# Kernel optimization log

Hardware: AMD Instinct MI355X
Metric: run time of the kernel (lower is better)

The kernel has to match this reference:

```python
import jax, jax.numpy as jnp
import numpy as np

B, S, DIM = 2, 2048, 2048
H, DH = 16, 128
FF = 4 * DIM
EPS = 1e-5


def layer_norm(x, w, b, eps=EPS):
    m = jnp.mean(x, axis=-1, keepdims=True)
    v = jnp.mean(jnp.square(x - m), axis=-1, keepdims=True)
    return (x - m) * jax.lax.rsqrt(v + eps) * w + b


def apply_rotary(x, cos, sin):
    # x: [B, H, S, DH]; cos/sin: [S, DH//2]; complex multiply on (even, odd) pairs
    x2 = x.reshape(*x.shape[:-1], DH // 2, 2)
    x0, x1 = x2[..., 0], x2[..., 1]
    c = cos[None, None, :, :]
    s = sin[None, None, :, :]
    r0 = x0 * c - x1 * s
    r1 = x0 * s + x1 * c
    return jnp.stack([r0, r1], axis=-1).reshape(x.shape)


def setup_inputs() -> dict:
    key = jax.random.key(0)
    ks = jax.random.split(key, 16)
    sc = 0.02
    pos = jnp.arange(S, dtype=jnp.float32)[:, None]
    inv_freq = 1.0 / (10000.0 ** (jnp.arange(0, DH // 2, dtype=jnp.float32) / (DH // 2)))
    ang = pos * inv_freq[None, :]
    return {
        "hidden_states": jax.random.normal(ks[0], (B, S, DIM), jnp.float32),
        "freqs_cos": jnp.cos(ang),
        "freqs_sin": jnp.sin(ang),
        "wq": jax.random.normal(ks[1], (DIM, H * DH), jnp.float32) * sc,
        "wk": jax.random.normal(ks[2], (DIM, H * DH), jnp.float32) * sc,
        "wv": jax.random.normal(ks[3], (DIM, H * DH), jnp.float32) * sc,
        "nq_w": jnp.ones((DH,), jnp.float32),
        "nq_b": jnp.zeros((DH,), jnp.float32),
        "nk_w": jnp.ones((DH,), jnp.float32),
        "nk_b": jnp.zeros((DH,), jnp.float32),
        "wo": jax.random.normal(ks[4], (H * DH, DIM), jnp.float32) * sc,
        "bo": jnp.zeros((DIM,), jnp.float32),
        "ln1_w": jnp.ones((DIM,), jnp.float32),
        "ln1_b": jnp.zeros((DIM,), jnp.float32),
        "ln3_w": jnp.ones((DIM,), jnp.float32),
        "ln3_b": jnp.zeros((DIM,), jnp.float32),
        "w1": jax.random.normal(ks[5], (DIM, FF), jnp.float32) * sc,
        "b1": jnp.zeros((FF,), jnp.float32),
        "w2": jax.random.normal(ks[6], (FF, DIM), jnp.float32) * sc,
        "b2": jnp.zeros((DIM,), jnp.float32),
    }


def reference(hidden_states, freqs_cos, freqs_sin, wq, wk, wv, nq_w, nq_b, nk_w, nk_b,
              wo, bo, ln1_w, ln1_b, ln3_w, ln3_b, w1, b1, w2, b2):
    x = hidden_states
    # --- self-attention branch ---
    n = layer_norm(x, ln1_w, ln1_b)                       # [B,S,DIM]
    q = (n @ wq).reshape(B, S, H, DH)
    k = (n @ wk).reshape(B, S, H, DH)
    v = (n @ wv).reshape(B, S, H, DH)
    # per-head QK LayerNorm (norm over dim_head)
    q = layer_norm(q, nq_w, nq_b)
    k = layer_norm(k, nk_w, nk_b)
    q = q.transpose(0, 2, 1, 3)                            # [B,H,S,DH]
    k = k.transpose(0, 2, 1, 3)
    v = v.transpose(0, 2, 1, 3)
    q = apply_rotary(q, freqs_cos, freqs_sin)
    k = apply_rotary(k, freqs_cos, freqs_sin)
    scale = DH ** -0.5
    scores = jnp.einsum("bhqd,bhkd->bhqk", q, k) * scale   # [B,H,S,S]
    probs = jax.nn.softmax(scores, axis=-1)
    attn = jnp.einsum("bhqk,bhkd->bhqd", probs, v)         # [B,H,S,DH]
    attn = attn.transpose(0, 2, 1, 3).reshape(B, S, H * DH)
    x = x + (attn @ wo + bo)
    # --- feed-forward branch ---
    n = layer_norm(x, ln3_w, ln3_b)
    h = jax.nn.gelu(n @ w1 + b1, approximate=False)
    x = x + (h @ w2 + b2)
    return x
```

## Files before the change

### kernel.cpp

```cpp
#include <hip/hip_runtime.h>
#include <hip/hip_bf16.h>
#include <stdint.h>

typedef __hip_bfloat16 bf16;
typedef float v4f __attribute__((ext_vector_type(4)));
typedef short v8s __attribute__((ext_vector_type(8)));

#define DEV __device__ __forceinline__

DEV float b2f(bf16 x) { return __bfloat162float(x); }
DEV bf16 f2b(float x) { return __float2bfloat16(x); }

DEV void load4(const float* p, float* f) {
  float4 t = *(const float4*)p;
  f[0] = t.x; f[1] = t.y; f[2] = t.z; f[3] = t.w;
}
DEV void load4(const bf16* p, float* f) {
  union { uint2 u; bf16 h[4]; } t;
  t.u = *(const uint2*)p;
#pragma unroll
  for (int i = 0; i < 4; i++) f[i] = b2f(t.h[i]);
}
DEV void load8(const float* p, float* f) {
  float4 a = ((const float4*)p)[0], b = ((const float4*)p)[1];
  f[0] = a.x; f[1] = a.y; f[2] = a.z; f[3] = a.w;
  f[4] = b.x; f[5] = b.y; f[6] = b.z; f[7] = b.w;
}
DEV void load8(const bf16* p, float* f) {
  union { uint4 u; bf16 h[8]; } t;
  t.u = *(const uint4*)p;
#pragma unroll
  for (int i = 0; i < 8; i++) f[i] = b2f(t.h[i]);
}
DEV void store4(bf16* p, const float* f) {
  union { uint2 u; bf16 h[4]; } t;
#pragma unroll
  for (int i = 0; i < 4; i++) t.h[i] = f2b(f[i]);
  *(uint2*)p = t.u;
}
DEV void store4(float* p, const float* f) {
  *(float4*)p = make_float4(f[0], f[1], f[2], f[3]);
}

DEV void gld_lds16(const bf16* g, bf16* l) {
  auto gp = reinterpret_cast<const __attribute__((address_space(1))) uint32_t*>(
      reinterpret_cast<uintptr_t>(g));
  auto lp = reinterpret_cast<__attribute__((address_space(3))) uint32_t*>(
      reinterpret_cast<uintptr_t>(l));
  __builtin_amdgcn_global_load_lds(gp, lp, 16, 0, 0);
}

template <typename XT>
__global__ __launch_bounds__(256)
void ln2048_kernel(const XT* __restrict__ x, const float* __restrict__ w,
                   const float* __restrict__ b, bf16* __restrict__ y) {
  const int N = 2048;
  int row = blockIdx.x, tid = threadIdx.x;
  const XT* xr = x + (size_t)row * N;
  bf16* yr = y + (size_t)row * N;
  float f[8], s = 0.f, ss = 0.f;
  load8(xr + tid * 8, f);
#pragma unroll
  for (int i = 0; i < 8; i++) { s += f[i]; ss += f[i] * f[i]; }
#pragma unroll
  for (int off = 32; off >= 1; off >>= 1) {
    s  += __shfl_xor(s, off, 64);
    ss += __shfl_xor(ss, off, 64);
  }
  __shared__ float red0[4], red1[4];
  int wv = tid >> 6;
  if ((tid & 63) == 0) { red0[wv] = s; red1[wv] = ss; }
  __syncthreads();
  s  = red0[0] + red0[1] + red0[2] + red0[3];
  ss = red1[0] + red1[1] + red1[2] + red1[3];
  float mean = s * (1.f / N);
  float var  = ss * (1.f / N) - mean * mean;
  float inv  = rsqrtf(var + 1e-5f);
  float wf[8], bf_[8];
  load8(w + tid * 8, wf);
  load8(b + tid * 8, bf_);
  union { uint4 u; bf16 h[8]; } vo;
#pragma unroll
  for (int i = 0; i < 8; i++)
    vo.h[i] = f2b((f[i] - mean) * inv * wf[i] + bf_[i]);
  ((uint4*)yr)[tid] = vo.u;
}

__global__ __launch_bounds__(256)
void headln_rope_kernel(bf16* __restrict__ q, const float* __restrict__ w,
                        const float* __restrict__ b, const float* __restrict__ fcos,
                        const float* __restrict__ fsin) {
  int tid = threadIdx.x;
  int wv = tid >> 6, ln = tid & 63;
  int idx = blockIdx.x * 4 + wv;
  int row = idx >> 4, h = idx & 15;
  int srow = row & 2047;
  bf16* p = q + (size_t)row * 2048 + h * 128 + ln * 2;
  union { unsigned int u; bf16 h2[2]; } v;
  v.u = *(const unsigned int*)p;
  float x0 = b2f(v.h2[0]), x1 = b2f(v.h2[1]);
  float s = x0 + x1, ss = x0 * x0 + x1 * x1;
#pragma unroll
  for (int off = 32; off >= 1; off >>= 1) {
    s  += __shfl_xor(s, off, 64);
    ss += __shfl_xor(ss, off, 64);
  }
  float mean = s * (1.f / 128.f);
  float var  = ss * (1.f / 128.f) - mean * mean;
  float inv  = rsqrtf(var + 1e-5f);
  float w0 = w[ln * 2], w1 = w[ln * 2 + 1];
  float b0 = b[ln * 2], b1 = b[ln * 2 + 1];
  x0 = (x0 - mean) * inv * w0 + b0;
  x1 = (x1 - mean) * inv * w1 + b1;
  float c  = fcos[srow * 64 + ln];
  float sn = fsin[srow * 64 + ln];
  v.h2[0] = f2b(x0 * c - x1 * sn);
  v.h2[1] = f2b(x0 * sn + x1 * c);
  *(unsigned int*)p = v.u;
}

__global__ __launch_bounds__(256)
void convT_kernel(const float* __restrict__ src, bf16* __restrict__ dst,
                  int K, int N) {
  __shared__ float T[64][65];
  int n0 = blockIdx.x * 64, k0 = blockIdx.y * 64;
  int t = threadIdx.x;
  int tr = t >> 4, tc4 = (t & 15) * 4;
#pragma unroll
  for (int it = 0; it < 4; it++) {
    float4 v = *(const float4*)&src[(size_t)(k0 + tr + 16 * it) * N + n0 + tc4];
    T[tr + 16 * it][tc4 + 0] = v.x;
    T[tr + 16 * it][tc4 + 1] = v.y;
    T[tr + 16 * it][tc4 + 2] = v.z;
    T[tr + 16 * it][tc4 + 3] = v.w;
  }
  __syncthreads();
#pragma unroll
  for (int it = 0; it < 4; it++) {
    int n = tr + 16 * it;
    union { uint2 u; bf16 h[4]; } o;
#pragma unroll
    for (int c = 0; c < 4; c++) o.h[c] = f2b(T[tc4 + c][n]);
    *(uint2*)&dst[(size_t)(n0 + n) * K + k0 + tc4] = o.u;
  }
}

template <int EPI, typename RT, typename OT>
__global__ __launch_bounds__(256, 2)
void mfma_gemm_kernel(const bf16* __restrict__ A, const bf16* __restrict__ BT,
                      OT* __restrict__ C, const float* __restrict__ bias,
                      const RT* __restrict__ res, int M, int N, int K) {
  __shared__ __align__(16) bf16 As[128 * 32];
  __shared__ __align__(16) bf16 Bs[128 * 32];
  int tid = threadIdx.x;
  int lane = tid & 63, wave = tid >> 6;
  int wr = wave >> 1, wc = wave & 1;
  int m0 = blockIdx.y * 128, n0 = blockIdx.x * 128;

  int ls_row = lane >> 2;
  int ls_k   = (lane & 3) * 8;
  int t0 = 2 * wave, t1 = 2 * wave + 1;
  const bf16* gA0 = A  + (size_t)(m0 + 16 * t0 + ls_row) * K + ls_k;
  const bf16* gA1 = A  + (size_t)(m0 + 16 * t1 + ls_row) * K + ls_k;
  const bf16* gB0 = BT + (size_t)(n0 + 16 * t0 + ls_row) * K + ls_k;
  const bf16* gB1 = BT + (size_t)(n0 + 16 * t1 + ls_row) * K + ls_k;
  bf16* lA0 = As + t0 * 512;
  bf16* lA1 = As + t1 * 512;
  bf16* lB0 = Bs + t0 * 512;
  bf16* lB1 = Bs + t1 * 512;

  int fr = lane & 15, fk = (lane >> 4) * 8;
  const bf16* pA = As + (wr * 64 + fr) * 32 + fk;
  const bf16* pB = Bs + (wc * 64 + fr) * 32 + fk;

  v4f acc[4][4];
#pragma unroll
  for (int i = 0; i < 4; i++)
#pragma unroll
    for (int j = 0; j < 4; j++) acc[i][j] = (v4f){0.f, 0.f, 0.f, 0.f};

  for (int k0 = 0; k0 < K; k0 += 32) {
    __syncthreads();
    gld_lds16(gA0, lA0); gld_lds16(gA1, lA1);
    gld_lds16(gB0, lB0); gld_lds16(gB1, lB1);
    gA0 += 32; gA1 += 32; gB0 += 32; gB1 += 32;
    __syncthreads();
    v8s af[4], bfr[4];
#pragma unroll
    for (int i = 0; i < 4; i++) af[i]  = *(const v8s*)(pA + i * 16 * 32);
#pragma unroll
    for (int j = 0; j < 4; j++) bfr[j] = *(const v8s*)(pB + j * 16 * 32);
#pragma unroll
    for (int i = 0; i < 4; i++)
#pragma unroll
      for (int j = 0; j < 4; j++)
        acc[i][j] = __builtin_amdgcn_mfma_f32_16x16x32_bf16(af[i], bfr[j],
                                                            acc[i][j], 0, 0, 0);
  }

  int rq = (lane >> 4) * 4;
#pragma unroll
  for (int j = 0; j < 4; j++) {
    int n = n0 + wc * 64 + j * 16 + (lane & 15);
    float bb = (EPI >= 1) ? bias[n] : 0.f;
#pragma unroll
    for (int i = 0; i < 4; i++) {
#pragma unroll
      for (int r = 0; r < 4; r++) {
        int m = m0 + wr * 64 + i * 16 + rq + r;
        float val = acc[i][j][r] + bb;
        if (EPI == 2)
          val = 0.5f * val * (1.f + erff(val * 0.70710678118654752f));
        if (EPI == 1) {
          if constexpr (__is_same(RT, float)) val += res[(size_t)m * N + n];
          else                                val += b2f(res[(size_t)m * N + n]);
        }
        if constexpr (__is_same(OT, float)) C[(size_t)m * N + n] = val;
        else                                C[(size_t)m * N + n] = f2b(val);
      }
    }
  }
}

template <int EPI, typename RT, typename OT>
__global__ __launch_bounds__(256)
void gemm_kernel(const bf16* __restrict__ A, const float* __restrict__ Bm,
                 OT* __restrict__ C, const float* __restrict__ bias,
                 const RT* __restrict__ res, int M, int N, int K) {
  const int BK = 32;
  __shared__ __align__(16) float As[BK][68];
  __shared__ __align__(16) float Bs[BK][68];
  int tid = threadIdx.x;
  int bm = blockIdx.y, bn = blockIdx.x;
  int tx = tid & 15, ty = tid >> 4;
  int am = tid >> 2, ak8 = (tid & 3) * 8;
  int bkr = tid >> 3, bn8 = (tid & 7) * 8;
  const bf16* Aptr = A + (size_t)(bm * 64 + am) * K + ak8;
  const float* Bptr = Bm + (size_t)bkr * N + bn * 64 + bn8;
  float acc[4][4] = {};
  for (int k0 = 0; k0 < K; k0 += BK) {
    float av[8], bv[8];
    load8(Aptr, av);
    load8(Bptr, bv);
    __syncthreads();
#pragma unroll
    for (int j = 0; j < 8; j++) As[ak8 + j][am] = av[j];
#pragma unroll
    for (int j = 0; j < 8; j++) Bs[bkr][bn8 + j] = bv[j];
    __syncthreads();
    Aptr += BK;
    Bptr += (size_t)BK * N;
#pragma unroll 8
    for (int kk = 0; kk < BK; kk++) {
      float a0[4], b0[4];
      *(float4*)a0 = *(const float4*)&As[kk][ty * 4];
      *(float4*)b0 = *(const float4*)&Bs[kk][tx * 4];
#pragma unroll
      for (int i = 0; i < 4; i++)
#pragma unroll
        for (int j = 0; j < 4; j++)
          acc[i][j] += a0[i] * b0[j];
    }
  }
  int m0 = bm * 64 + ty * 4, n0 = bn * 64 + tx * 4;
#pragma unroll
  for (int i = 0; i < 4; i++) {
    float r4[4];
#pragma unroll
    for (int j = 0; j < 4; j++) r4[j] = acc[i][j];
    if (EPI >= 1) {
      float bb[4];
      load4(bias + n0, bb);
#pragma unroll
      for (int j = 0; j < 4; j++) r4[j] += bb[j];
    }
    if (EPI == 2) {
#pragma unroll
      for (int j = 0; j < 4; j++)
        r4[j] = 0.5f * r4[j] * (1.f + erff(r4[j] * 0.70710678118654752f));
    }
    if (EPI == 1) {
      float rr[4];
      load4(res + (size_t)(m0 + i) * N + n0, rr);
#pragma unroll
      for (int j = 0; j < 4; j++) r4[j] += rr[j];
    }
    store4(&C[(size_t)(m0 + i) * N + n0], r4);
  }
}

#define VSWZ(r) (((((r) >> 3) ^ (r)) & 7) << 4)

__global__ __launch_bounds__(256, 2)
void attn_kernel(const bf16* __restrict__ q, const bf16* __restrict__ k,
                 const bf16* __restrict__ v, bf16* __restrict__ o) {
  const int S = 2048, HD = 2048;
  __shared__ __align__(16) char smem[57856];
  char* Ks0 = smem;
  char* Ks1 = smem + 16384;
  char* VtB = smem + 32768;
  char* PB  = smem + 49152;
  float* Lp = (float*)(smem + 57344);

  int id = blockIdx.x;
  int swzb = (id & 7) * 128 + (id >> 3);
  int bh = swzb >> 5, qb = swzb & 31;
  int q0 = qb * 64;
  size_t base = (size_t)(bh >> 4) * S * HD + (size_t)(bh & 15) * 128;

  int tid = threadIdx.x;
  int lane = tid & 63, wave = tid >> 6;
  int wr = wave >> 1, wc = wave & 1;
  int fr = lane & 15, fg = lane >> 4;

  if (tid < 128) Lp[tid] = 0.f;

  union V4U { uint4 u; bf16 h[8]; };
  int vr0 = (tid & 15) * 4, vd0 = (tid >> 4) * 8;

#pragma unroll
  for (int t = 0; t < 4; t++) {
    int ti = wave * 4 + t;
    int r = ti * 4 + fg;
    int cb = (fr * 16) ^ ((r & 7) << 4);
    gld_lds16(q + base + (size_t)(q0 + r) * HD + (cb >> 1), (bf16*)Ks0 + ti * 512);
    gld_lds16(k + base + (size_t)r * HD + (cb >> 1), (bf16*)Ks1 + ti * 512);
  }
  V4U vA[4], vB[4];
#pragma unroll
  for (int j = 0; j < 4; j++)
    vA[j].u = *(const uint4*)&v[base + (size_t)(vr0 + j) * HD + vd0];
  __syncthreads();

  v8s qfrag[2][4];
#pragma unroll
  for (int i = 0; i < 2; i++)
#pragma unroll
    for (int kk = 0; kk < 4; kk++) {
      int row = wr * 32 + i * 16 + fr;
      int off = row * 256 + ((kk * 64 + fg * 16) ^ ((row & 7) << 4));
      qfrag[i][kk] = *(const v8s*)(Ks0 + off);
    }
  __syncthreads();

  v4f oacc[2][4];
#pragma unroll
  for (int i = 0; i < 2; i++)
#pragma unroll
    for (int j = 0; j < 4; j++) oacc[i][j] = (v4f){0.f, 0.f, 0.f, 0.f};

  const float scale = 0.08838834764831845f;

#define ATTN_TILE(KT, KCUR, KNXT, VCUR, VNXT, STAGE_NEXT)                     \
  {                                                                           \
    _Pragma("unroll")                                                         \
    for (int c = 0; c < 8; c++) {                                             \
      int d = vd0 + c;                                                        \
      union { uint2 u2; bf16 hh[4]; } pk;                                     \
      _Pragma("unroll")                                                       \
      for (int j = 0; j < 4; j++) pk.hh[j] = VCUR[j].h[c];                    \
      *(uint2*)(VtB + d * 128 + ((vr0 * 2) ^ VSWZ(d))) = pk.u2;               \
    }                                                                         \
    if (STAGE_NEXT) {                                                         \
      _Pragma("unroll")                                                       \
      for (int t = 0; t < 4; t++) {                                           \
        int ti = wave * 4 + t;                                                \
        int r = ti * 4 + fg;                                                  \
        int cb = (fr * 16) ^ ((r & 7) << 4);                                  \
        gld_lds16(k + base + (size_t)((KT) + 64 + r) * HD + (cb >> 1),        \
                  (bf16*)(KNXT) + ti * 512);                                  \
      }                                                                       \
      _Pragma("unroll")                                                       \
      for (int j = 0; j < 4; j++)                                             \
        VNXT[j].u =                                                           \
            *(const uint4*)&v[base + (size_t)((KT) + 64 + vr0 + j) * HD + vd0]; \
    }                                                                         \
    v4f sacc[2][2];                                                           \
    _Pragma("unroll")                                                         \
    for (int i = 0; i < 2; i++)                                               \
      _Pragma("unroll")                                                       \
      for (int j = 0; j < 2; j++) sacc[i][j] = (v4f){0.f, 0.f, 0.f, 0.f};     \
    __builtin_amdgcn_s_setprio(1);                                            \
    _Pragma("unroll")                                                         \
    for (int kk = 0; kk < 4; kk++) {                                          \
      v8s kf[2];                                                              \
      _Pragma("unroll")                                                       \
      for (int j = 0; j < 2; j++) {                                           \
        int row = wc * 32 + j * 16 + fr;                                      \
        int off = row * 256 + ((kk * 64 + fg * 16) ^ ((row & 7) << 4));       \
        kf[j] = *(const v8s*)((KCUR) + off);                                  \
      }                                                                       \
      _Pragma("unroll")                                                       \
      for (int i = 0; i < 2; i++)                                             \
        _Pragma("unroll")                                                     \
        for (int j = 0; j < 2; j++)                                           \
          sacc[i][j] = __builtin_amdgcn_mfma_f32_16x16x32_bf16(               \
              qfrag[i][kk], kf[j], sacc[i][j], 0, 0, 0);                      \
    }                                                                         \
    __builtin_amdgcn_s_setprio(0);                                            \
    _Pragma("unroll")                                                         \
    for (int i = 0; i < 2; i++)                                               \
      _Pragma("unroll")                                                       \
      for (int r = 0; r < 4; r++) {                                           \
        int qrow = wr * 32 + i * 16 + fg * 4 + r;                             \
        float e0 = __expf(sacc[i][0][r] * scale);                             \
        float e1 = __expf(sacc[i][1][r] * scale);                             \
        int sw = VSWZ(qrow);                                                  \
        int c0 = wc * 64 + fr * 2;                                            \
        *(bf16*)(PB + qrow * 128 + (c0 ^ sw)) = f2b(e0);                      \
        *(bf16*)(PB + qrow * 128 + ((c0 + 32) ^ sw)) = f2b(e1);               \
        float s_ = e0 + e1;                                                   \
        s_ += __shfl_xor(s_, 1, 64);                                          \
        s_ += __shfl_xor(s_, 2, 64);                                          \
        s_ += __shfl_xor(s_, 4, 64);                                          \
        s_ += __shfl_xor(s_, 8, 64);                                          \
        if (fr == 0) Lp[wc * 64 + qrow] += s_;                                \
      }                                                                       \
    __syncthreads();                                                          \
    __builtin_amdgcn_s_setprio(1);                                            \
    _Pragma("unroll")                                                         \
    for (int kk2 = 0; kk2 < 2; kk2++) {                                       \
      v8s pf[2], vf[4];                                                       \
      _Pragma("unroll")                                                       \
      for (int i = 0; i < 2; i++) {                                           \
        int row = wr * 32 + i * 16 + fr;                                      \
        int off = row * 128 + ((kk2 * 64 + fg * 16) ^ VSWZ(row));             \
        pf[i] = *(const v8s*)(PB + off);                                      \
      }                                                                       \
      _Pragma("unroll")                                                       \
      for (int j = 0; j < 4; j++) {                                           \
        int row = wc * 64 + j * 16 + fr;                                      \
        int off = row * 128 + ((kk2 * 64 + fg * 16) ^ VSWZ(row));             \
        vf[j] = *(const v8s*)(VtB + off);                                     \
      }                                                                       \
      _Pragma("unroll")                                                       \
      for (int i = 0; i < 2; i++)                                             \
        _Pragma("unroll")                                                     \
        for (int j = 0; j < 4; j++)                                           \
          oacc[i][j] = __builtin_amdgcn_mfma_f32_16x16x32_bf16(               \
              pf[i], vf[j], oacc[i][j], 0, 0, 0);                             \
    }                                                                         \
    __builtin_amdgcn_s_setprio(0);                                            \
    __syncthreads();                                                          \
  }

  for (int tp = 0; tp < 16; tp++) {
    int kt = tp * 128;
    ATTN_TILE(kt, Ks1, Ks0, vA, vB, true);
    ATTN_TILE(kt + 64, Ks0, Ks1, vB, vA, (tp < 15));
  }
#undef ATTN_TILE

#pragma unroll
  for (int i = 0; i < 2; i++)
#pragma unroll
    for (int r = 0; r < 4; r++) {
      int qrow = wr * 32 + i * 16 + fg * 4 + r;
      float linv = 1.f / (Lp[qrow] + Lp[64 + qrow]);
#pragma unroll
      for (int j = 0; j < 4; j++) {
        int d = wc * 64 + j * 16 + fr;
        o[base + (size_t)(q0 + qrow) * HD + d] = f2b(oacc[i][j][r] * linv);
      }
    }
}

extern "C" void kernel_launch(void* const* d_in, const int* in_sizes, int n_in,
                              void* d_out, int out_size, void* d_ws, size_t ws_size,
                              hipStream_t stream) {
  (void)in_sizes; (void)n_in; (void)out_size;
  const float* x    = (const float*)d_in[0];
  const float* fcos = (const float*)d_in[1];
  const float* fsin = (const float*)d_in[2];
  const float* wq   = (const float*)d_in[3];
  const float* wk   = (const float*)d_in[4];
  const float* wv   = (const float*)d_in[5];
  const float* nqw  = (const float*)d_in[6];
  const float* nqb  = (const float*)d_in[7];
  const float* nkw  = (const float*)d_in[8];
  const float* nkb  = (const float*)d_in[9];
  const float* wo   = (const float*)d_in[10];
  const float* bo   = (const float*)d_in[11];
  const float* ln1w = (const float*)d_in[12];
  const float* ln1b = (const float*)d_in[13];
  const float* ln3w = (const float*)d_in[14];
  const float* ln3b = (const float*)d_in[15];
  const float* w1   = (const float*)d_in[16];
  const float* b1   = (const float*)d_in[17];
  const float* w2   = (const float*)d_in[18];
  const float* b2   = (const float*)d_in[19];
  float* out = (float*)d_out;

  const size_t SEG = (size_t)4096 * 2048;
  bf16* base = (bf16*)d_ws;
  bf16* q        = base + 0 * SEG;
  bf16* k        = base + 1 * SEG;
  bf16* v        = base + 2 * SEG;
  bf16* n1       = base + 3 * SEG;
  bf16* attn_out = base + 3 * SEG;
  bf16* x2       = base + 4 * SEG;
  bf16* n3       = base + 5 * SEG;
  bf16* h        = base + 0 * SEG;

  dim3 blk(256);
  ln2048_kernel<float><<<4096, blk, 0, stream>>>(x, ln1w, ln1b, n1);

  bool mfma_path = ws_size >= (size_t)128 * 1024 * 1024;
  if (mfma_path) {
    bf16* W = base + 6 * SEG;
    bf16* wqT = W;
    bf16* wkT = W + 4 * 1024 * 1024;
    bf16* wvT = W + 8 * 1024 * 1024;
    bf16* woT = W;
    bf16* w1T = W;
    bf16* w2T = W;

    dim3 cg22(32, 32);
    dim3 g16(16, 32);
    dim3 g64(64, 32);

    convT_kernel<<<cg22, blk, 0, stream>>>(wq, wqT, 2048, 2048);
    convT_kernel<<<cg22, blk, 0, stream>>>(wk, wkT, 2048, 2048);
    convT_kernel<<<cg22, blk, 0, stream>>>(wv, wvT, 2048, 2048);
    mfma_gemm_kernel<0, float, bf16><<<g16, blk, 0, stream>>>(n1, wqT, q, nullptr, nullptr, 4096, 2048, 2048);
    mfma_gemm_kernel<0, float, bf16><<<g16, blk, 0, stream>>>(n1, wkT, k, nullptr, nullptr, 4096, 2048, 2048);
    mfma_gemm_kernel<0, float, bf16><<<g16, blk, 0, stream>>>(n1, wvT, v, nullptr, nullptr, 4096, 2048, 2048);
    headln_rope_kernel<<<16384, blk, 0, stream>>>(q, nqw, nqb, fcos, fsin);
    headln_rope_kernel<<<16384, blk, 0, stream>>>(k, nkw, nkb, fcos, fsin);
    attn_kernel<<<1024, blk, 0, stream>>>(q, k, v, attn_out);
    convT_kernel<<<cg22, blk, 0, stream>>>(wo, woT, 2048, 2048);
    mfma_gemm_kernel<1, float, bf16><<<g16, blk, 0, stream>>>(attn_out, woT, x2, bo, x, 4096, 2048, 2048);
    ln2048_kernel<bf16><<<4096, blk, 0, stream>>>(x2, ln3w, ln3b, n3);
    convT_kernel<<<dim3(128, 32), blk, 0, stream>>>(w1, w1T, 2048, 8192);
    mfma_gemm_kernel<2, float, bf16><<<g64, blk, 0, stream>>>(n3, w1T, h, b1, nullptr, 4096, 8192, 2048);
    convT_kernel<<<dim3(32, 128), blk, 0, stream>>>(w2, w2T, 8192, 2048);
    mfma_gemm_kernel<1, bf16, float><<<g16, blk, 0, stream>>>(h, w2T, out, b2, x2, 4096, 2048, 8192);
  } else {
    dim3 g2048(32, 64), g8192(128, 64);
    gemm_kernel<0, float, bf16><<<g2048, blk, 0, stream>>>(n1, wq, q, nullptr, nullptr, 4096, 2048, 2048);
    gemm_kernel<0, float, bf16><<<g2048, blk, 0, stream>>>(n1, wk, k, nullptr, nullptr, 4096, 2048, 2048);
    gemm_kernel<0, float, bf16><<<g2048, blk, 0, stream>>>(n1, wv, v, nullptr, nullptr, 4096, 2048, 2048);
    headln_rope_kernel<<<16384, blk, 0, stream>>>(q, nqw, nqb, fcos, fsin);
    headln_rope_kernel<<<16384, blk, 0, stream>>>(k, nkw, nkb, fcos, fsin);
    attn_kernel<<<1024, blk, 0, stream>>>(q, k, v, attn_out);
    gemm_kernel<1, float, bf16><<<g2048, blk, 0, stream>>>(attn_out, wo, x2, bo, x, 4096, 2048, 2048);
    ln2048_kernel<bf16><<<4096, blk, 0, stream>>>(x2, ln3w, ln3b, n3);
    gemm_kernel<2, float, bf16><<<g8192, blk, 0, stream>>>(n3, w1, h, b1, nullptr, 4096, 8192, 2048);
    gemm_kernel<1, bf16, float><<<g2048, blk, 0, stream>>>(h, w2, out, b2, x2, 4096, 2048, 8192);
  }
}
```

Before: 1.026 ms.

## Fuse QKV projections into one GEMM, merge q/k head-norm launches, swizzle tiles

Runs the Q, K and V projections as a single GEMM with N=6144 over the contiguous transposed weights, and scatters each output column into its separate q/k/v buffer using a segment stride. The two per-head LayerNorm+RoPE launches are merged into one launch that picks q or k by block index. The MFMA GEMM also remaps block IDs in groups of eight to improve L2 reuse. This cuts launch count and tail effects and raises occupancy for the projection, but it assumes wqT/wkT/wvT and q/k/v sit at fixed strides in the workspace.

```diff
diff --git a/kernel.cpp b/kernel.cpp
--- a/kernel.cpp
+++ b/kernel.cpp
@@ -87,15 +87,20 @@
 }
 
 __global__ __launch_bounds__(256)
-void headln_rope_kernel(bf16* __restrict__ q, const float* __restrict__ w,
-                        const float* __restrict__ b, const float* __restrict__ fcos,
-                        const float* __restrict__ fsin) {
+void headln_rope_kernel(bf16* __restrict__ qb, bf16* __restrict__ kb,
+                        const float* __restrict__ nqw, const float* __restrict__ nqb,
+                        const float* __restrict__ nkw, const float* __restrict__ nkb,
+                        const float* __restrict__ fcos, const float* __restrict__ fsin) {
+  int bid = blockIdx.x;
+  bf16* qk; const float* w; const float* b;
+  if (bid < 16384) { qk = qb; w = nqw; b = nqb; }
+  else             { qk = kb; w = nkw; b = nkb; bid -= 16384; }
   int tid = threadIdx.x;
   int wv = tid >> 6, ln = tid & 63;
-  int idx = blockIdx.x * 4 + wv;
+  int idx = bid * 4 + wv;
   int row = idx >> 4, h = idx & 15;
   int srow = row & 2047;
-  bf16* p = q + (size_t)row * 2048 + h * 128 + ln * 2;
+  bf16* p = qk + (size_t)row * 2048 + h * 128 + ln * 2;
   union { unsigned int u; bf16 h2[2]; } v;
   v.u = *(const unsigned int*)p;
   float x0 = b2f(v.h2[0]), x1 = b2f(v.h2[1]);
@@ -149,13 +154,20 @@
 __global__ __launch_bounds__(256, 2)
 void mfma_gemm_kernel(const bf16* __restrict__ A, const bf16* __restrict__ BT,
                       OT* __restrict__ C, const float* __restrict__ bias,
-                      const RT* __restrict__ res, int M, int N, int K) {
+                      const RT* __restrict__ res, int M, int N, int K,
+                      int ldc_log2, size_t seg_stride) {
   __shared__ __align__(16) bf16 As[128 * 32];
   __shared__ __align__(16) bf16 Bs[128 * 32];
   int tid = threadIdx.x;
   int lane = tid & 63, wave = tid >> 6;
   int wr = wave >> 1, wc = wave & 1;
-  int m0 = blockIdx.y * 128, n0 = blockIdx.x * 128;
+
+  int nbx = gridDim.x;
+  int bid = blockIdx.y * nbx + blockIdx.x;
+  int nwg = nbx * gridDim.y;
+  int cpx = nwg >> 3;
+  int swz = (bid & 7) * cpx + (bid >> 3);
+  int m0 = (swz / nbx) * 128, n0 = (swz % nbx) * 128;
 
   int ls_row = lane >> 2;
   int ls_k   = (lane & 3) * 8;
@@ -199,10 +211,12 @@
   }
 
   int rq = (lane >> 4) * 4;
+  int ldm = 1 << ldc_log2;
 #pragma unroll
   for (int j = 0; j < 4; j++) {
     int n = n0 + wc * 64 + j * 16 + (lane & 15);
     float bb = (EPI >= 1) ? bias[n] : 0.f;
+    size_t cseg = (size_t)(n >> ldc_log2) * seg_stride + (n & (ldm - 1));
 #pragma unroll
     for (int i = 0; i < 4; i++) {
 #pragma unroll
@@ -215,8 +229,9 @@
           if constexpr (__is_same(RT, float)) val += res[(size_t)m * N + n];
           else                                val += b2f(res[(size_t)m * N + n]);
         }
-        if constexpr (__is_same(OT, float)) C[(size_t)m * N + n] = val;
-        else                                C[(size_t)m * N + n] = f2b(val);
+        size_t cix = cseg + ((size_t)m << ldc_log2);
+        if constexpr (__is_same(OT, float)) C[cix] = val;
+        else                                C[cix] = f2b(val);
       }
     }
   }
@@ -517,31 +532,28 @@
 
     dim3 cg22(32, 32);
     dim3 g16(16, 32);
+    dim3 g48(48, 32);
     dim3 g64(64, 32);
 
     convT_kernel<<<cg22, blk, 0, stream>>>(wq, wqT, 2048, 2048);
     convT_kernel<<<cg22, blk, 0, stream>>>(wk, wkT, 2048, 2048);
     convT_kernel<<<cg22, blk, 0, stream>>>(wv, wvT, 2048, 2048);
-    mfma_gemm_kernel<0, float, bf16><<<g16, blk, 0, stream>>>(n1, wqT, q, nullptr, nullptr, 4096, 2048, 2048);
-    mfma_gemm_kernel<0, float, bf16><<<g16, blk, 0, stream>>>(n1, wkT, k, nullptr, nullptr, 4096, 2048, 2048);
-    mfma_gemm_kernel<0, float, bf16><<<g16, blk, 0, stream>>>(n1, wvT, v, nullptr, nullptr, 4096, 2048, 2048);
-    headln_rope_kernel<<<16384, blk, 0, stream>>>(q, nqw, nqb, fcos, fsin);
-    headln_rope_kernel<<<16384, blk, 0, stream>>>(k, nkw, nkb, fcos, fsin);
+    mfma_gemm_kernel<0, float, bf16><<<g48, blk, 0, stream>>>(n1, wqT, q, nullptr, nullptr, 4096, 6144, 2048, 11, SEG);
+    headln_rope_kernel<<<32768, blk, 0, stream>>>(q, k, nqw, nqb, nkw, nkb, fcos, fsin);
     attn_kernel<<<1024, blk, 0, stream>>>(q, k, v, attn_out);
     convT_kernel<<<cg22, blk, 0, stream>>>(wo, woT, 2048, 2048);
-    mfma_gemm_kernel<1, float, bf16><<<g16, blk, 0, stream>>>(attn_out, woT, x2, bo, x, 4096, 2048, 2048);
+    mfma_gemm_kernel<1, float, bf16><<<g16, blk, 0, stream>>>(attn_out, woT, x2, bo, x, 4096, 2048, 2048, 11, 0);
     ln2048_kernel<bf16><<<4096, blk, 0, stream>>>(x2, ln3w, ln3b, n3);
     convT_kernel<<<dim3(128, 32), blk, 0, stream>>>(w1, w1T, 2048, 8192);
-    mfma_gemm_kernel<2, float, bf16><<<g64, blk, 0, stream>>>(n3, w1T, h, b1, nullptr, 4096, 8192, 2048);
+    mfma_gemm_kernel<2, float, bf16><<<g64, blk, 0, stream>>>(n3, w1T, h, b1, nullptr, 4096, 8192, 2048, 13, 0);
     convT_kernel<<<dim3(32, 128), blk, 0, stream>>>(w2, w2T, 8192, 2048);
-    mfma_gemm_kernel<1, bf16, float><<<g16, blk, 0, stream>>>(h, w2T, out, b2, x2, 4096, 2048, 8192);
+    mfma_gemm_kernel<1, bf16, float><<<g16, blk, 0, stream>>>(h, w2T, out, b2, x2, 4096, 2048, 8192, 11, 0);
   } else {
     dim3 g2048(32, 64), g8192(128, 64);
     gemm_kernel<0, float, bf16><<<g2048, blk, 0, stream>>>(n1, wq, q, nullptr, nullptr, 4096, 2048, 2048);
     gemm_kernel<0, float, bf16><<<g2048, blk, 0, stream>>>(n1, wk, k, nullptr, nullptr, 4096, 2048, 2048);
     gemm_kernel<0, float, bf16><<<g2048, blk, 0, stream>>>(n1, wv, v, nullptr, nullptr, 4096, 2048, 2048);
-    headln_rope_kernel<<<16384, blk, 0, stream>>>(q, nqw, nqb, fcos, fsin);
-    headln_rope_kernel<<<16384, blk, 0, stream>>>(k, nkw, nkb, fcos, fsin);
+    headln_rope_kernel<<<32768, blk, 0, stream>>>(q, k, nqw, nqb, nkw, nkb, fcos, fsin);
     attn_kernel<<<1024, blk, 0, stream>>>(q, k, v, attn_out);
     gemm_kernel<1, float, bf16><<<g2048, blk, 0, stream>>>(attn_out, wo, x2, bo, x, 4096, 2048, 2048);
     ln2048_kernel<bf16><<<4096, blk, 0, stream>>>(x2, ln3w, ln3b, n3);
```

Result: no change. 1.018 ms (-0.8%).
